# Kernel tuning notes

Hardware: AMD Instinct MI355X
Metric: run time of the kernel (lower is better)

The kernel has to match this reference:

```python
import jax, jax.numpy as jnp
import numpy as np

DIM = 256


def setup_inputs() -> dict:
    key = jax.random.key(0)
    ks = jax.random.split(key, 10)
    d = DIM
    inp = {
        "agent": jax.random.normal(ks[0], (64, d), dtype=jnp.float32),
        "x": jax.random.normal(ks[1], (8, 4096, d), dtype=jnp.float32),
        # parameters (stored as [in, out]; y = x @ W + b)
        "W_qkv": jax.random.normal(ks[2], (d, 3 * d), dtype=jnp.float32) * (d ** -0.5),
        "b_qkv": jnp.zeros((3 * d,), dtype=jnp.float32),
        "W_agent": jax.random.normal(ks[3], (d, 2 * d), dtype=jnp.float32) * (d ** -0.5),
        "b_agent": jnp.zeros((2 * d,), dtype=jnp.float32),
        "W_fc1": jax.random.normal(ks[4], (d, d), dtype=jnp.float32) * (d ** -0.5),
        "b_fc1": jnp.zeros((d,), dtype=jnp.float32),
        "W_fc2": jax.random.normal(ks[5], (d, d), dtype=jnp.float32) * (d ** -0.5),
        "b_fc2": jnp.zeros((d,), dtype=jnp.float32),
    }
    return inp


def reference(agent, x, W_qkv, b_qkv, W_agent, b_agent, W_fc1, b_fc1, W_fc2, b_fc2):
    d = x.shape[-1]
    scale = d ** -0.5
    # qkv projection of tokens: [B,N,3d] -> q,k,v each [B,N,d]
    qkv = x @ W_qkv + b_qkv
    q, k, v = jnp.split(qkv, 3, axis=-1)
    # agent projection: [K,2d] -> q_agent,k_agent each [K,d]
    ag = agent @ W_agent + b_agent
    q_agent, k_agent = jnp.split(ag, 2, axis=-1)
    # stage 1: agents attend over tokens -> [B,K,N]
    attn1 = jax.nn.softmax(jnp.einsum('kd,bnd->bkn', q_agent, k) * scale, axis=-1)
    va = jnp.einsum('bkn,bnd->bkd', attn1, v)  # [B,K,d]
    va = va @ W_fc1 + b_fc1
    # stage 2: tokens attend over agents -> [B,N,K]
    attn2 = jax.nn.softmax(jnp.einsum('bnd,kd->bnk', q, k_agent) * scale, axis=-1)
    out = jnp.einsum('bnk,bkd->bnd', attn2, va)  # [B,N,d]
    out = out @ W_fc2 + b_fc2
    return out + x
```

## Files before the change

### kernel.cpp

```cpp
#include <hip/hip_runtime.h>
#include <stdint.h>
#include <string.h>

#define BB 8
#define NN 4096
#define DD 256
#define QS 512
#define SCALE 0.0625f

using frag_ab = __attribute__((ext_vector_type(8))) short;
using frag_cd = __attribute__((ext_vector_type(4))) float;

__device__ __forceinline__ unsigned short f2bf(float f) {
    union { float f; unsigned u; } a; a.f = f;
    unsigned r = a.u + 0x7FFFu + ((a.u >> 16) & 1u);
    return (unsigned short)(r >> 16);
}

__global__ __launch_bounds__(256) void k_xconv(
    const float* __restrict__ x, unsigned short* __restrict__ xb)
{
    size_t idx = (size_t)blockIdx.x * 1024 + threadIdx.x * 4;
    float4 v = *(const float4*)&x[idx];
    unsigned short u[4] = {f2bf(v.x), f2bf(v.y), f2bf(v.z), f2bf(v.w)};
    uint2 pk; memcpy(&pk, u, 8);
    *(uint2*)&xb[idx] = pk;
}

__global__ __launch_bounds__(256) void k_setup(
    const float* __restrict__ Wqkv, unsigned short* __restrict__ Wt,
    const float* __restrict__ agent, const float* __restrict__ Wag,
    const float* __restrict__ bag, unsigned short* __restrict__ agb,
    const float* __restrict__ Wfc1, const float* __restrict__ Wfc2,
    const float* __restrict__ bfc1, float* __restrict__ W12, float* __restrict__ b12)
{
    __shared__ float sh[64 * 65];
    const int bx = blockIdx.x, tid = threadIdx.x;
    if (bx < 48) {
        const int n0 = (bx % 12) * 64, k0 = (bx / 12) * 64;
#pragma unroll
        for (int p = 0; p < 16; ++p) {
            int idx = p * 256 + tid;
            int k = idx >> 6, n = idx & 63;
            sh[k * 65 + n] = Wqkv[(k0 + k) * 768 + n0 + n];
        }
        __syncthreads();
#pragma unroll
        for (int p = 0; p < 16; ++p) {
            int idx = p * 256 + tid;
            int n = idx >> 6, k = idx & 63;
            Wt[(size_t)(n0 + n) * 256 + k0 + k] = f2bf(sh[k * 65 + n]);
        }
    } else if (bx < 112) {
        const int row = bx - 48;
        sh[tid] = agent[row * 256 + tid];
        __syncthreads();
#pragma unroll
        for (int h = 0; h < 2; ++h) {
            int j = tid + h * 256;
            float s = bag[j];
            for (int kk = 0; kk < 256; ++kk) s += sh[kk] * Wag[kk * 512 + j];
            agb[row * 512 + j] = f2bf(s);
        }
    } else {
        const int i = bx - 112, j = tid;
        float s = 0.f;
        for (int k = 0; k < 256; ++k) s += Wfc1[i * 256 + k] * Wfc2[k * 256 + j];
        W12[i * 256 + j] = s;
        if (i == 0) {
            float t = 0.f;
            for (int k = 0; k < 256; ++k) t += bfc1[k] * Wfc2[k * 256 + j];
            b12[j] = t;
        }
    }
}

__global__ __launch_bounds__(256) void k_qkv_mfma(
    const unsigned short* __restrict__ xb, const unsigned short* __restrict__ Wt,
    const float* __restrict__ bqkv, unsigned short* __restrict__ qkv,
    unsigned short* __restrict__ VT)
{
    __shared__ unsigned short lds[2 * 128 * 72];
    unsigned short* As = lds;
    unsigned short* Bs = lds + 128 * 72;
    const int m0 = blockIdx.x * 128;
    const int n0 = blockIdx.y * 128;
    const int tid = threadIdx.x;
    const int wave = tid >> 6, lane = tid & 63;
    const int ml = lane & 15, q = lane >> 4;
    const int wm = (wave & 1) * 64, wn = (wave >> 1) * 64;

    frag_cd acc[4][4];
#pragma unroll
    for (int i = 0; i < 4; ++i)
#pragma unroll
        for (int j = 0; j < 4; ++j)
#pragma unroll
            for (int r = 0; r < 4; ++r) acc[i][j][r] = 0.f;

    for (int kb = 0; kb < 256; kb += 64) {
        __syncthreads();
#pragma unroll
        for (int p = 0; p < 4; ++p) {
            int idx = p * 256 + tid;
            int r = idx >> 3, c = (idx & 7) * 8;
            *(uint4*)&As[r * 72 + c] =
                *(const uint4*)&xb[(size_t)(m0 + r) * 256 + kb + c];
            *(uint4*)&Bs[r * 72 + c] =
                *(const uint4*)&Wt[(size_t)(n0 + r) * 256 + kb + c];
        }
        __syncthreads();
#pragma unroll
        for (int ks = 0; ks < 2; ++ks) {
            const int kk = ks * 32 + q * 8;
            frag_ab a[4], b[4];
#pragma unroll
            for (int i = 0; i < 4; ++i)
                a[i] = *(const frag_ab*)&As[(wm + i * 16 + ml) * 72 + kk];
#pragma unroll
            for (int j = 0; j < 4; ++j)
                b[j] = *(const frag_ab*)&Bs[(wn + j * 16 + ml) * 72 + kk];
#pragma unroll
            for (int i = 0; i < 4; ++i)
#pragma unroll
                for (int j = 0; j < 4; ++j)
                    acc[i][j] = __builtin_amdgcn_mfma_f32_16x16x32_bf16(
                        a[i], b[j], acc[i][j], 0, 0, 0);
        }
    }

    float bias[4];
#pragma unroll
    for (int j = 0; j < 4; ++j) bias[j] = bqkv[n0 + wn + j * 16 + ml];

    if (n0 >= 512) {
        const int b = m0 >> 12;
        const int tok0 = (m0 & 4095) + wm;
        const int d0 = n0 - 512 + wn;
#pragma unroll
        for (int i = 0; i < 4; ++i)
#pragma unroll
            for (int j = 0; j < 4; ++j) {
                unsigned short u[4];
#pragma unroll
                for (int r = 0; r < 4; ++r) u[r] = f2bf(acc[i][j][r] + bias[j]);
                uint2 pk; memcpy(&pk, u, 8);
                *(uint2*)&VT[(size_t)(b * 256 + d0 + j * 16 + ml) * 4096 +
                             tok0 + i * 16 + q * 4] = pk;
            }
    } else {
        __syncthreads();
        unsigned short* E = lds + wave * 64 * 72;
#pragma unroll
        for (int i = 0; i < 4; ++i)
#pragma unroll
            for (int j = 0; j < 4; ++j)
#pragma unroll
                for (int r = 0; r < 4; ++r)
                    E[(i * 16 + q * 4 + r) * 72 + j * 16 + ml] =
                        f2bf(acc[i][j][r] + bias[j]);
        __syncthreads();
#pragma unroll
        for (int p = 0; p < 8; ++p) {
            int idx = p * 64 + lane;
            int r = idx >> 3, c = (idx & 7) * 8;
            *(uint4*)&qkv[(size_t)(m0 + wm + r) * QS + n0 + wn + c] =
                *(const uint4*)&E[r * 72 + c];
        }
    }
}

__global__ __launch_bounds__(256) void k_logits1_stats(
    const unsigned short* __restrict__ agb, const unsigned short* __restrict__ qkv,
    float* __restrict__ attn1, float* __restrict__ statM, float* __restrict__ statS)
{
    __shared__ unsigned short As[64 * 72];
    __shared__ unsigned short Bs[64 * 72];
    __shared__ float Sm[4][64], Ss[4][64], Cm[64];
    const int chunk = blockIdx.x;
    const int n0 = chunk * 64;
    const int b = blockIdx.y;
    const int tid = threadIdx.x;
    const int w = tid >> 6, lane = tid & 63;
    const int ml = lane & 15, q = lane >> 4;

    frag_cd acc[4];
#pragma unroll
    for (int j = 0; j < 4; ++j)
#pragma unroll
        for (int r = 0; r < 4; ++r) acc[j][r] = 0.f;

    for (int kb = 0; kb < 256; kb += 64) {
        __syncthreads();
#pragma unroll
        for (int p = 0; p < 2; ++p) {
            int idx = p * 256 + tid;
            int r = idx >> 3, c = (idx & 7) * 8;
            *(uint4*)&As[r * 72 + c] =
                *(const uint4*)&qkv[(size_t)(b * 4096 + n0 + r) * QS + 256 + kb + c];
            *(uint4*)&Bs[r * 72 + c] = *(const uint4*)&agb[r * 512 + kb + c];
        }
        __syncthreads();
#pragma unroll
        for (int ks = 0; ks < 2; ++ks) {
            const int kk = ks * 32 + q * 8;
            frag_ab a = *(const frag_ab*)&As[(w * 16 + ml) * 72 + kk];
#pragma unroll
            for (int j = 0; j < 4; ++j) {
                frag_ab bf = *(const frag_ab*)&Bs[(j * 16 + ml) * 72 + kk];
                acc[j] = __builtin_amdgcn_mfma_f32_16x16x32_bf16(a, bf, acc[j], 0, 0, 0);
            }
        }
    }

    float l[4][4];
#pragma unroll
    for (int j = 0; j < 4; ++j) {
        int ag = j * 16 + ml;
#pragma unroll
        for (int r = 0; r < 4; ++r) l[j][r] = acc[j][r] * SCALE;
        float4 o = make_float4(l[j][0], l[j][1], l[j][2], l[j][3]);
        *(float4*)&attn1[(size_t)(b * 64 + ag) * 4096 + n0 + w * 16 + q * 4] = o;
    }
#pragma unroll
    for (int j = 0; j < 4; ++j) {
        float m = fmaxf(fmaxf(l[j][0], l[j][1]), fmaxf(l[j][2], l[j][3]));
        m = fmaxf(m, __shfl_xor(m, 16));
        m = fmaxf(m, __shfl_xor(m, 32));
        if (q == 0) Sm[w][j * 16 + ml] = m;
    }
    __syncthreads();
    if (tid < 64)
        Cm[tid] = fmaxf(fmaxf(Sm[0][tid], Sm[1][tid]), fmaxf(Sm[2][tid], Sm[3][tid]));
    __syncthreads();
#pragma unroll
    for (int j = 0; j < 4; ++j) {
        float cm = Cm[j * 16 + ml];
        float s = __expf(l[j][0] - cm) + __expf(l[j][1] - cm) +
                  __expf(l[j][2] - cm) + __expf(l[j][3] - cm);
        s += __shfl_xor(s, 16);
        s += __shfl_xor(s, 32);
        if (q == 0) Ss[w][j * 16 + ml] = s;
    }
    __syncthreads();
    if (tid < 64) {
        float s = Ss[0][tid] + Ss[1][tid] + Ss[2][tid] + Ss[3][tid];
        size_t idx = (size_t)(b * 64 + tid) * 64 + chunk;
        statM[idx] = Cm[tid];
        statS[idx] = s;
    }
}

__global__ __launch_bounds__(256) void k_va_fused(
    const float* __restrict__ attn1, const float* __restrict__ statM,
    const float* __restrict__ statS, const unsigned short* __restrict__ VT,
    float* __restrict__ part)
{
    __shared__ unsigned short As[64 * 144];
    __shared__ unsigned short Bs[128 * 144];
    __shared__ float rowM[64], rowInv[64];
    const int s = blockIdx.x, dh = blockIdx.y, b = blockIdx.z;
    const int tid = threadIdx.x;
    const int w = tid >> 6, lane = tid & 63;
    const int ml = lane & 15, q = lane >> 4;

    if (tid < 64) {
        const float* pm = &statM[(size_t)(b * 64 + tid) * 64];
        const float* ps = &statS[(size_t)(b * 64 + tid) * 64];
        float m = -INFINITY;
#pragma unroll 8
        for (int c = 0; c < 64; ++c) m = fmaxf(m, pm[c]);
        float sum = 0.f;
#pragma unroll 8
        for (int c = 0; c < 64; ++c) sum += ps[c] * __expf(pm[c] - m);
        rowM[tid] = m;
        rowInv[tid] = 1.f / sum;
    }
#pragma unroll
    for (int p = 0; p < 8; ++p) {
        int idx = p * 256 + tid;
        int r = idx >> 4, c = (idx & 15) * 8;
        *(uint4*)&Bs[r * 144 + c] =
            *(const uint4*)&VT[(size_t)(b * 256 + dh * 128 + r) * 4096 + s * 128 + c];
    }
    __syncthreads();
#pragma unroll
    for (int p = 0; p < 32; ++p) {
        int idx = p * 256 + tid;
        int ag = idx >> 7, t = idx & 127;
        float l = attn1[(size_t)(b * 64 + ag) * 4096 + s * 128 + t];
        As[ag * 144 + t] = f2bf(__expf(l - rowM[ag]) * rowInv[ag]);
    }
    __syncthreads();

    frag_cd acc[4][2];
#pragma unroll
    for (int i = 0; i < 4; ++i)
#pragma unroll
        for (int j = 0; j < 2; ++j)
#pragma unroll
            for (int r = 0; r < 4; ++r) acc[i][j][r] = 0.f;
#pragma unroll
    for (int ks = 0; ks < 4; ++ks) {
        const int kk = ks * 32 + q * 8;
        frag_ab a[4];
#pragma unroll
        for (int i = 0; i < 4; ++i)
            a[i] = *(const frag_ab*)&As[(i * 16 + ml) * 144 + kk];
#pragma unroll
        for (int j = 0; j < 2; ++j) {
            frag_ab bf = *(const frag_ab*)&Bs[(w * 32 + j * 16 + ml) * 144 + kk];
#pragma unroll
            for (int i = 0; i < 4; ++i)
                acc[i][j] = __builtin_amdgcn_mfma_f32_16x16x32_bf16(
                    a[i], bf, acc[i][j], 0, 0, 0);
        }
    }
#pragma unroll
    for (int i = 0; i < 4; ++i)
#pragma unroll
        for (int j = 0; j < 2; ++j) {
            int d = dh * 128 + w * 32 + j * 16 + ml;
#pragma unroll
            for (int r = 0; r < 4; ++r)
                part[(size_t)((s * 8 + b) * 64 + i * 16 + q * 4 + r) * 256 + d] =
                    acc[i][j][r];
        }
}

__global__ __launch_bounds__(256) void k_fc(
    const float* __restrict__ part, const float* __restrict__ W12,
    const float* __restrict__ b12, unsigned short* __restrict__ va3t)
{
    __shared__ float rowb[256];
    const int row = blockIdx.x, tid = threadIdx.x;
    const int b = row >> 6, ag = row & 63;
    float sv = 0.f;
    for (int s = 0; s < 32; ++s)
        sv += part[(size_t)((s * 8 + b) * 64 + ag) * 256 + tid];
    rowb[tid] = sv;
    __syncthreads();
    float s2 = b12[tid];
    for (int k = 0; k < 256; ++k) s2 += rowb[k] * W12[k * 256 + tid];
    va3t[(size_t)(b * 256 + tid) * 64 + ag] = f2bf(s2);
}

__global__ __launch_bounds__(256) void k_stage2_mfma(
    const unsigned short* __restrict__ qkv, const unsigned short* __restrict__ agb,
    const unsigned short* __restrict__ va3t, const float* __restrict__ x,
    const float* __restrict__ bfc2, float* __restrict__ out)
{
    __shared__ unsigned short As[64 * 72];
    __shared__ unsigned short Bs[64 * 72];
    __shared__ unsigned short Vs[256 * 72];
    const int n0 = blockIdx.x * 64;
    const int b = blockIdx.y;
    const int tid = threadIdx.x;
    const int w = tid >> 6, lane = tid & 63;
    const int ml = lane & 15, q = lane >> 4;

#pragma unroll
    for (int p = 0; p < 8; ++p) {
        int idx = p * 256 + tid;
        int r = idx >> 3, c = (idx & 7) * 8;
        *(uint4*)&Vs[r * 72 + c] = *(const uint4*)&va3t[(size_t)(b * 256 + r) * 64 + c];
    }

    frag_cd acc1[4];
#pragma unroll
    for (int j = 0; j < 4; ++j)
#pragma unroll
        for (int r = 0; r < 4; ++r) acc1[j][r] = 0.f;

    for (int kb = 0; kb < 256; kb += 64) {
        __syncthreads();
#pragma unroll
        for (int p = 0; p < 2; ++p) {
            int idx = p * 256 + tid;
            int r = idx >> 3, c = (idx & 7) * 8;
            *(uint4*)&As[r * 72 + c] =
                *(const uint4*)&qkv[(size_t)(b * 4096 + n0 + r) * QS + kb + c];
            *(uint4*)&Bs[r * 72 + c] = *(const uint4*)&agb[r * 512 + 256 + kb + c];
        }
        __syncthreads();
#pragma unroll
        for (int ks = 0; ks < 2; ++ks) {
            const int kk = ks * 32 + q * 8;
            frag_ab a = *(const frag_ab*)&As[(w * 16 + ml) * 72 + kk];
#pragma unroll
            for (int j = 0; j < 4; ++j) {
                frag_ab bf = *(const frag_ab*)&Bs[(j * 16 + ml) * 72 + kk];
                acc1[j] = __builtin_amdgcn_mfma_f32_16x16x32_bf16(a, bf, acc1[j], 0, 0, 0);
            }
        }
    }

    unsigned short* Ps = As;
#pragma unroll
    for (int r = 0; r < 4; ++r) {
        float v0 = acc1[0][r] * SCALE, v1 = acc1[1][r] * SCALE;
        float v2 = acc1[2][r] * SCALE, v3 = acc1[3][r] * SCALE;
        float m = fmaxf(fmaxf(v0, v1), fmaxf(v2, v3));
#pragma unroll
        for (int mask = 1; mask <= 8; mask <<= 1) m = fmaxf(m, __shfl_xor(m, mask));
        float e0 = __expf(v0 - m), e1 = __expf(v1 - m);
        float e2 = __expf(v2 - m), e3 = __expf(v3 - m);
        float sm = e0 + e1 + e2 + e3;
#pragma unroll
        for (int mask = 1; mask <= 8; mask <<= 1) sm += __shfl_xor(sm, mask);
        float inv = 1.f / sm;
        int trow = w * 16 + q * 4 + r;
        Ps[trow * 72 + 0 * 16 + ml] = f2bf(e0 * inv);
        Ps[trow * 72 + 1 * 16 + ml] = f2bf(e1 * inv);
        Ps[trow * 72 + 2 * 16 + ml] = f2bf(e2 * inv);
        Ps[trow * 72 + 3 * 16 + ml] = f2bf(e3 * inv);
    }
    __syncthreads();

    frag_cd acc2[4][4];
#pragma unroll
    for (int i = 0; i < 4; ++i)
#pragma unroll
        for (int j = 0; j < 4; ++j)
#pragma unroll
            for (int r = 0; r < 4; ++r) acc2[i][j][r] = 0.f;
#pragma unroll
    for (int ks = 0; ks < 2; ++ks) {
        const int kk = ks * 32 + q * 8;
        frag_ab bf[4];
#pragma unroll
        for (int j = 0; j < 4; ++j)
            bf[j] = *(const frag_ab*)&Vs[(w * 64 + j * 16 + ml) * 72 + kk];
#pragma unroll
        for (int i = 0; i < 4; ++i) {
            frag_ab a = *(const frag_ab*)&Ps[(i * 16 + ml) * 72 + kk];
#pragma unroll
            for (int j = 0; j < 4; ++j)
                acc2[i][j] = __builtin_amdgcn_mfma_f32_16x16x32_bf16(
                    a, bf[j], acc2[i][j], 0, 0, 0);
        }
    }

    float bias[4];
#pragma unroll
    for (int j = 0; j < 4; ++j) bias[j] = bfc2[w * 64 + j * 16 + ml];
#pragma unroll
    for (int i = 0; i < 4; ++i) {
        size_t base = ((size_t)b * 4096 + n0 + i * 16 + q * 4) * 256;
#pragma unroll
        for (int j = 0; j < 4; ++j) {
            int d = w * 64 + j * 16 + ml;
#pragma unroll
            for (int r = 0; r < 4; ++r) {
                size_t a = base + (size_t)r * 256 + d;
                out[a] = acc2[i][j][r] + bias[j] + x[a];
            }
        }
    }
}

extern "C" void kernel_launch(void* const* d_in, const int* in_sizes, int n_in,
                              void* d_out, int out_size, void* d_ws, size_t ws_size,
                              hipStream_t stream) {
    const float* agent = (const float*)d_in[0];
    const float* x     = (const float*)d_in[1];
    const float* Wqkv  = (const float*)d_in[2];
    const float* bqkv  = (const float*)d_in[3];
    const float* Wag   = (const float*)d_in[4];
    const float* bag   = (const float*)d_in[5];
    const float* Wfc1  = (const float*)d_in[6];
    const float* bfc1  = (const float*)d_in[7];
    const float* Wfc2  = (const float*)d_in[8];
    const float* bfc2  = (const float*)d_in[9];
    float* out = (float*)d_out;

    char* w = (char*)d_ws;
    size_t off = 0;
    unsigned short* qkv = (unsigned short*)(w + off); off += (size_t)BB * NN * QS * 2;
    unsigned short* VT  = (unsigned short*)(w + off); off += (size_t)BB * DD * NN * 2;
    unsigned short* agb = (unsigned short*)(w + off); off += (size_t)64 * 512 * 2;
    float* attn1 = (float*)(w + off); off += (size_t)BB * 64 * NN * 4;
    float* statM = (float*)(w + off); off += (size_t)BB * 64 * 64 * 4;
    float* statS = (float*)(w + off); off += (size_t)BB * 64 * 64 * 4;
    float* W12 = (float*)(w + off); off += (size_t)256 * 256 * 4;
    float* b12 = (float*)(w + off); off += 4096;
    unsigned short* va3t = (unsigned short*)(w + off); off += (size_t)BB * DD * 64 * 2;
    unsigned short* Wt = (unsigned short*)(w + off); off += (size_t)768 * DD * 2;
    char* shared = w + off; off += (size_t)32 * BB * 64 * 256 * 4;
    unsigned short* xb = (unsigned short*)shared;
    float* part = (float*)shared;

    k_xconv<<<8192, 256, 0, stream>>>(x, xb);
    k_setup<<<368, 256, 0, stream>>>(Wqkv, Wt, agent, Wag, bag, agb,
                                     Wfc1, Wfc2, bfc1, W12, b12);
    k_qkv_mfma<<<dim3(256, 6), 256, 0, stream>>>(xb, Wt, bqkv, qkv, VT);
    k_logits1_stats<<<dim3(64, 8), 256, 0, stream>>>(agb, qkv, attn1, statM, statS);
    k_va_fused<<<dim3(32, 2, 8), 256, 0, stream>>>(attn1, statM, statS, VT, part);
    k_fc<<<512, 256, 0, stream>>>(part, W12, b12, va3t);
    k_stage2_mfma<<<dim3(64, 8), 256, 0, stream>>>(qkv, agb, va3t, x, bfc2, out);
}
```

Measured before the change: 199.3 us.

## Eliminate token QKV projection by folding weights into agent-side matrices

Rewrites the pipeline algebraically so the large x@W_qkv GEMM is never computed. Agent queries and keys are pre-multiplied by the q and k weight slices, giving one 128-column matrix that turns x directly into both attention logit sets. W_v is folded into fc1 and fc2, so stage 1 aggregates raw x. This removes the big projection and its q/k/v buffers, at the cost of a transposed bf16 copy of x and writing stage-2 logits to memory as fp32.

```diff
diff --git a/kernel.cpp b/kernel.cpp
--- a/kernel.cpp
+++ b/kernel.cpp
@@ -5,7 +5,6 @@
 #define BB 8
 #define NN 4096
 #define DD 256
-#define QS 512
 #define SCALE 0.0625f
 
 using frag_ab = __attribute__((ext_vector_type(8))) short;
@@ -17,178 +16,130 @@
     return (unsigned short)(r >> 16);
 }
 
-__global__ __launch_bounds__(256) void k_xconv(
-    const float* __restrict__ x, unsigned short* __restrict__ xb)
-{
-    size_t idx = (size_t)blockIdx.x * 1024 + threadIdx.x * 4;
-    float4 v = *(const float4*)&x[idx];
-    unsigned short u[4] = {f2bf(v.x), f2bf(v.y), f2bf(v.z), f2bf(v.w)};
-    uint2 pk; memcpy(&pk, u, 8);
-    *(uint2*)&xb[idx] = pk;
-}
-
-__global__ __launch_bounds__(256) void k_setup(
-    const float* __restrict__ Wqkv, unsigned short* __restrict__ Wt,
+__global__ __launch_bounds__(256) void k_xprep(
+    const float* __restrict__ x, unsigned short* __restrict__ xb,
+    unsigned short* __restrict__ xt)
+{
+    __shared__ float T[64 * 65];
+    const int n0 = blockIdx.x * 64, d0 = blockIdx.y * 64, b = blockIdx.z;
+    const int tid = threadIdx.x;
+#pragma unroll
+    for (int p = 0; p < 16; ++p) {
+        int idx = p * 256 + tid;
+        int n = idx >> 6, d = idx & 63;
+        T[n * 65 + d] = x[(size_t)(b * 4096 + n0 + n) * 256 + d0 + d];
+    }
+    __syncthreads();
+#pragma unroll
+    for (int p = 0; p < 16; ++p) {
+        int idx = p * 256 + tid;
+        int n = idx >> 6, d = idx & 63;
+        xb[(size_t)(b * 4096 + n0 + n) * 256 + d0 + d] = f2bf(T[n * 65 + d]);
+    }
+#pragma unroll
+    for (int p = 0; p < 16; ++p) {
+        int idx = p * 256 + tid;
+        int d = idx >> 6, n = idx & 63;
+        xt[(size_t)(b * 256 + d0 + d) * 4096 + n0 + n] = f2bf(T[n * 65 + d]);
+    }
+}
+
+__global__ __launch_bounds__(256) void k_setup1(
     const float* __restrict__ agent, const float* __restrict__ Wag,
-    const float* __restrict__ bag, unsigned short* __restrict__ agb,
-    const float* __restrict__ Wfc1, const float* __restrict__ Wfc2,
-    const float* __restrict__ bfc1, float* __restrict__ W12, float* __restrict__ b12)
-{
-    __shared__ float sh[64 * 65];
+    const float* __restrict__ bag, float* __restrict__ ag,
+    const float* __restrict__ Wqkv, const float* __restrict__ Wfc1,
+    const float* __restrict__ bqkv, const float* __restrict__ bfc1,
+    float* __restrict__ T, float* __restrict__ Tb)
+{
+    __shared__ float sh[256];
     const int bx = blockIdx.x, tid = threadIdx.x;
-    if (bx < 48) {
-        const int n0 = (bx % 12) * 64, k0 = (bx / 12) * 64;
-#pragma unroll
-        for (int p = 0; p < 16; ++p) {
-            int idx = p * 256 + tid;
-            int k = idx >> 6, n = idx & 63;
-            sh[k * 65 + n] = Wqkv[(k0 + k) * 768 + n0 + n];
-        }
-        __syncthreads();
-#pragma unroll
-        for (int p = 0; p < 16; ++p) {
-            int idx = p * 256 + tid;
-            int n = idx >> 6, k = idx & 63;
-            Wt[(size_t)(n0 + n) * 256 + k0 + k] = f2bf(sh[k * 65 + n]);
-        }
-    } else if (bx < 112) {
-        const int row = bx - 48;
-        sh[tid] = agent[row * 256 + tid];
+    if (bx < 64) {
+        sh[tid] = agent[bx * 256 + tid];
         __syncthreads();
 #pragma unroll
         for (int h = 0; h < 2; ++h) {
             int j = tid + h * 256;
             float s = bag[j];
             for (int kk = 0; kk < 256; ++kk) s += sh[kk] * Wag[kk * 512 + j];
-            agb[row * 512 + j] = f2bf(s);
+            ag[bx * 512 + j] = s;
         }
     } else {
-        const int i = bx - 112, j = tid;
+        const int i = bx - 64;
+        sh[tid] = Wqkv[i * 768 + 512 + tid];
+        __syncthreads();
         float s = 0.f;
-        for (int k = 0; k < 256; ++k) s += Wfc1[i * 256 + k] * Wfc2[k * 256 + j];
-        W12[i * 256 + j] = s;
+        for (int o = 0; o < 256; ++o) s += sh[o] * Wfc1[o * 256 + tid];
+        T[i * 256 + tid] = s;
+        if (i == 0) {
+            float t = bfc1[tid];
+            for (int o = 0; o < 256; ++o) t += bqkv[512 + o] * Wfc1[o * 256 + tid];
+            Tb[tid] = t;
+        }
+    }
+}
+
+__global__ __launch_bounds__(256) void k_setup2(
+    const float* __restrict__ ag, const float* __restrict__ Wqkv,
+    const float* __restrict__ bqkv, unsigned short* __restrict__ P12t,
+    float* __restrict__ c12, const float* __restrict__ T,
+    const float* __restrict__ Tb, const float* __restrict__ Wfc2,
+    float* __restrict__ W3, float* __restrict__ b3)
+{
+    __shared__ float arow[256];
+    __shared__ float red[256];
+    const int bx = blockIdx.x, tid = threadIdx.x;
+    if (bx < 128) {
+        const int c = bx;
+        const int woff = (c < 64) ? 256 : 0;
+        const int aoff = (c < 64) ? 0 : 256;
+        const int row = c & 63;
+        arow[tid] = ag[row * 512 + aoff + tid];
+        __syncthreads();
+        float s = 0.f;
+        for (int o = 0; o < 256; ++o) s += Wqkv[tid * 768 + woff + o] * arow[o];
+        P12t[(size_t)c * 256 + tid] = f2bf(SCALE * s);
+        red[tid] = bqkv[woff + tid] * arow[tid];
+        __syncthreads();
+        for (int st = 128; st; st >>= 1) {
+            if (tid < st) red[tid] += red[tid + st];
+            __syncthreads();
+        }
+        if (tid == 0) c12[c] = SCALE * red[0];
+    } else {
+        const int i = bx - 128;
+        arow[tid] = T[i * 256 + tid];
+        __syncthreads();
+        float s = 0.f;
+        for (int k = 0; k < 256; ++k) s += arow[k] * Wfc2[k * 256 + tid];
+        W3[i * 256 + tid] = s;
         if (i == 0) {
             float t = 0.f;
-            for (int k = 0; k < 256; ++k) t += bfc1[k] * Wfc2[k * 256 + j];
-            b12[j] = t;
-        }
-    }
-}
-
-__global__ __launch_bounds__(256) void k_qkv_mfma(
-    const unsigned short* __restrict__ xb, const unsigned short* __restrict__ Wt,
-    const float* __restrict__ bqkv, unsigned short* __restrict__ qkv,
-    unsigned short* __restrict__ VT)
-{
-    __shared__ unsigned short lds[2 * 128 * 72];
-    unsigned short* As = lds;
-    unsigned short* Bs = lds + 128 * 72;
-    const int m0 = blockIdx.x * 128;
-    const int n0 = blockIdx.y * 128;
-    const int tid = threadIdx.x;
-    const int wave = tid >> 6, lane = tid & 63;
-    const int ml = lane & 15, q = lane >> 4;
-    const int wm = (wave & 1) * 64, wn = (wave >> 1) * 64;
-
-    frag_cd acc[4][4];
-#pragma unroll
-    for (int i = 0; i < 4; ++i)
-#pragma unroll
-        for (int j = 0; j < 4; ++j)
-#pragma unroll
-            for (int r = 0; r < 4; ++r) acc[i][j][r] = 0.f;
-
-    for (int kb = 0; kb < 256; kb += 64) {
-        __syncthreads();
-#pragma unroll
-        for (int p = 0; p < 4; ++p) {
-            int idx = p * 256 + tid;
-            int r = idx >> 3, c = (idx & 7) * 8;
-            *(uint4*)&As[r * 72 + c] =
-                *(const uint4*)&xb[(size_t)(m0 + r) * 256 + kb + c];
-            *(uint4*)&Bs[r * 72 + c] =
-                *(const uint4*)&Wt[(size_t)(n0 + r) * 256 + kb + c];
-        }
-        __syncthreads();
-#pragma unroll
-        for (int ks = 0; ks < 2; ++ks) {
-            const int kk = ks * 32 + q * 8;
-            frag_ab a[4], b[4];
-#pragma unroll
-            for (int i = 0; i < 4; ++i)
-                a[i] = *(const frag_ab*)&As[(wm + i * 16 + ml) * 72 + kk];
-#pragma unroll
-            for (int j = 0; j < 4; ++j)
-                b[j] = *(const frag_ab*)&Bs[(wn + j * 16 + ml) * 72 + kk];
-#pragma unroll
-            for (int i = 0; i < 4; ++i)
-#pragma unroll
-                for (int j = 0; j < 4; ++j)
-                    acc[i][j] = __builtin_amdgcn_mfma_f32_16x16x32_bf16(
-                        a[i], b[j], acc[i][j], 0, 0, 0);
-        }
-    }
-
-    float bias[4];
-#pragma unroll
-    for (int j = 0; j < 4; ++j) bias[j] = bqkv[n0 + wn + j * 16 + ml];
-
-    if (n0 >= 512) {
-        const int b = m0 >> 12;
-        const int tok0 = (m0 & 4095) + wm;
-        const int d0 = n0 - 512 + wn;
-#pragma unroll
-        for (int i = 0; i < 4; ++i)
-#pragma unroll
-            for (int j = 0; j < 4; ++j) {
-                unsigned short u[4];
-#pragma unroll
-                for (int r = 0; r < 4; ++r) u[r] = f2bf(acc[i][j][r] + bias[j]);
-                uint2 pk; memcpy(&pk, u, 8);
-                *(uint2*)&VT[(size_t)(b * 256 + d0 + j * 16 + ml) * 4096 +
-                             tok0 + i * 16 + q * 4] = pk;
-            }
-    } else {
-        __syncthreads();
-        unsigned short* E = lds + wave * 64 * 72;
-#pragma unroll
-        for (int i = 0; i < 4; ++i)
-#pragma unroll
-            for (int j = 0; j < 4; ++j)
-#pragma unroll
-                for (int r = 0; r < 4; ++r)
-                    E[(i * 16 + q * 4 + r) * 72 + j * 16 + ml] =
-                        f2bf(acc[i][j][r] + bias[j]);
-        __syncthreads();
-#pragma unroll
-        for (int p = 0; p < 8; ++p) {
-            int idx = p * 64 + lane;
-            int r = idx >> 3, c = (idx & 7) * 8;
-            *(uint4*)&qkv[(size_t)(m0 + wm + r) * QS + n0 + wn + c] =
-                *(const uint4*)&E[r * 72 + c];
-        }
-    }
-}
-
-__global__ __launch_bounds__(256) void k_logits1_stats(
-    const unsigned short* __restrict__ agb, const unsigned short* __restrict__ qkv,
-    float* __restrict__ attn1, float* __restrict__ statM, float* __restrict__ statS)
+            for (int k = 0; k < 256; ++k) t += Tb[k] * Wfc2[k * 256 + tid];
+            b3[tid] = t;
+        }
+    }
+}
+
+__global__ __launch_bounds__(256) void k_logits(
+    const unsigned short* __restrict__ xb, const unsigned short* __restrict__ P12t,
+    const float* __restrict__ c12, float* __restrict__ l1, float* __restrict__ l2,
+    float* __restrict__ statM, float* __restrict__ statS)
 {
     __shared__ unsigned short As[64 * 72];
-    __shared__ unsigned short Bs[64 * 72];
-    __shared__ float Sm[4][64], Ss[4][64], Cm[64];
-    const int chunk = blockIdx.x;
+    __shared__ unsigned short Bs[128 * 72];
+    const int chunk = blockIdx.x, b = blockIdx.y;
     const int n0 = chunk * 64;
-    const int b = blockIdx.y;
     const int tid = threadIdx.x;
     const int w = tid >> 6, lane = tid & 63;
     const int ml = lane & 15, q = lane >> 4;
 
-    frag_cd acc[4];
-#pragma unroll
-    for (int j = 0; j < 4; ++j)
-#pragma unroll
-        for (int r = 0; r < 4; ++r) acc[j][r] = 0.f;
+    frag_cd acc[4][2];
+#pragma unroll
+    for (int i = 0; i < 4; ++i)
+#pragma unroll
+        for (int j = 0; j < 2; ++j)
+#pragma unroll
+            for (int r = 0; r < 4; ++r) acc[i][j][r] = 0.f;
 
     for (int kb = 0; kb < 256; kb += 64) {
         __syncthreads();
@@ -197,63 +148,88 @@
             int idx = p * 256 + tid;
             int r = idx >> 3, c = (idx & 7) * 8;
             *(uint4*)&As[r * 72 + c] =
-                *(const uint4*)&qkv[(size_t)(b * 4096 + n0 + r) * QS + 256 + kb + c];
-            *(uint4*)&Bs[r * 72 + c] = *(const uint4*)&agb[r * 512 + kb + c];
+                *(const uint4*)&xb[(size_t)(b * 4096 + n0 + r) * 256 + kb + c];
+        }
+#pragma unroll
+        for (int p = 0; p < 4; ++p) {
+            int idx = p * 256 + tid;
+            int r = idx >> 3, c = (idx & 7) * 8;
+            *(uint4*)&Bs[r * 72 + c] =
+                *(const uint4*)&P12t[(size_t)r * 256 + kb + c];
         }
         __syncthreads();
 #pragma unroll
         for (int ks = 0; ks < 2; ++ks) {
             const int kk = ks * 32 + q * 8;
-            frag_ab a = *(const frag_ab*)&As[(w * 16 + ml) * 72 + kk];
-#pragma unroll
-            for (int j = 0; j < 4; ++j) {
-                frag_ab bf = *(const frag_ab*)&Bs[(j * 16 + ml) * 72 + kk];
-                acc[j] = __builtin_amdgcn_mfma_f32_16x16x32_bf16(a, bf, acc[j], 0, 0, 0);
+            frag_ab a[4], bf[2];
+#pragma unroll
+            for (int i = 0; i < 4; ++i)
+                a[i] = *(const frag_ab*)&As[(i * 16 + ml) * 72 + kk];
+#pragma unroll
+            for (int j = 0; j < 2; ++j)
+                bf[j] = *(const frag_ab*)&Bs[(w * 32 + j * 16 + ml) * 72 + kk];
+#pragma unroll
+            for (int i = 0; i < 4; ++i)
+#pragma unroll
+                for (int j = 0; j < 2; ++j)
+                    acc[i][j] = __builtin_amdgcn_mfma_f32_16x16x32_bf16(
+                        a[i], bf[j], acc[i][j], 0, 0, 0);
+        }
+    }
+
+    float cc[2];
+#pragma unroll
+    for (int j = 0; j < 2; ++j) cc[j] = c12[w * 32 + j * 16 + ml];
+
+    if (w < 2) {
+#pragma unroll
+        for (int j = 0; j < 2; ++j) {
+            const int agc = w * 32 + j * 16 + ml;
+            float l[4][4];
+            float m = -INFINITY;
+#pragma unroll
+            for (int i = 0; i < 4; ++i)
+#pragma unroll
+                for (int r = 0; r < 4; ++r) {
+                    l[i][r] = acc[i][j][r] + cc[j];
+                    m = fmaxf(m, l[i][r]);
+                }
+            m = fmaxf(m, __shfl_xor(m, 16));
+            m = fmaxf(m, __shfl_xor(m, 32));
+            float s = 0.f;
+#pragma unroll
+            for (int i = 0; i < 4; ++i)
+#pragma unroll
+                for (int r = 0; r < 4; ++r) s += __expf(l[i][r] - m);
+            s += __shfl_xor(s, 16);
+            s += __shfl_xor(s, 32);
+            if (q == 0) {
+                size_t si = (size_t)(b * 64 + agc) * 64 + chunk;
+                statM[si] = m;
+                statS[si] = s;
             }
-        }
-    }
-
-    float l[4][4];
-#pragma unroll
-    for (int j = 0; j < 4; ++j) {
-        int ag = j * 16 + ml;
-#pragma unroll
-        for (int r = 0; r < 4; ++r) l[j][r] = acc[j][r] * SCALE;
-        float4 o = make_float4(l[j][0], l[j][1], l[j][2], l[j][3]);
-        *(float4*)&attn1[(size_t)(b * 64 + ag) * 4096 + n0 + w * 16 + q * 4] = o;
-    }
-#pragma unroll
-    for (int j = 0; j < 4; ++j) {
-        float m = fmaxf(fmaxf(l[j][0], l[j][1]), fmaxf(l[j][2], l[j][3]));
-        m = fmaxf(m, __shfl_xor(m, 16));
-        m = fmaxf(m, __shfl_xor(m, 32));
-        if (q == 0) Sm[w][j * 16 + ml] = m;
-    }
-    __syncthreads();
-    if (tid < 64)
-        Cm[tid] = fmaxf(fmaxf(Sm[0][tid], Sm[1][tid]), fmaxf(Sm[2][tid], Sm[3][tid]));
-    __syncthreads();
-#pragma unroll
-    for (int j = 0; j < 4; ++j) {
-        float cm = Cm[j * 16 + ml];
-        float s = __expf(l[j][0] - cm) + __expf(l[j][1] - cm) +
-                  __expf(l[j][2] - cm) + __expf(l[j][3] - cm);
-        s += __shfl_xor(s, 16);
-        s += __shfl_xor(s, 32);
-        if (q == 0) Ss[w][j * 16 + ml] = s;
-    }
-    __syncthreads();
-    if (tid < 64) {
-        float s = Ss[0][tid] + Ss[1][tid] + Ss[2][tid] + Ss[3][tid];
-        size_t idx = (size_t)(b * 64 + tid) * 64 + chunk;
-        statM[idx] = Cm[tid];
-        statS[idx] = s;
+#pragma unroll
+            for (int i = 0; i < 4; ++i)
+                *(float4*)&l1[(size_t)(b * 64 + agc) * 4096 + n0 + i * 16 + q * 4] =
+                    make_float4(l[i][0], l[i][1], l[i][2], l[i][3]);
+        }
+    } else {
+#pragma unroll
+        for (int j = 0; j < 2; ++j) {
+            const int agc = (w - 2) * 32 + j * 16 + ml;
+#pragma unroll
+            for (int i = 0; i < 4; ++i)
+#pragma unroll
+                for (int r = 0; r < 4; ++r)
+                    l2[(size_t)(b * 4096 + n0 + i * 16 + q * 4 + r) * 64 + agc] =
+                        acc[i][j][r] + cc[j];
+        }
     }
 }
 
 __global__ __launch_bounds__(256) void k_va_fused(
-    const float* __restrict__ attn1, const float* __restrict__ statM,
-    const float* __restrict__ statS, const unsigned short* __restrict__ VT,
+    const float* __restrict__ l1, const float* __restrict__ statM,
+    const float* __restrict__ statS, const unsigned short* __restrict__ xt,
     float* __restrict__ part)
 {
     __shared__ unsigned short As[64 * 144];
@@ -281,15 +257,15 @@
         int idx = p * 256 + tid;
         int r = idx >> 4, c = (idx & 15) * 8;
         *(uint4*)&Bs[r * 144 + c] =
-            *(const uint4*)&VT[(size_t)(b * 256 + dh * 128 + r) * 4096 + s * 128 + c];
+            *(const uint4*)&xt[(size_t)(b * 256 + dh * 128 + r) * 4096 + s * 128 + c];
     }
     __syncthreads();
 #pragma unroll
     for (int p = 0; p < 32; ++p) {
         int idx = p * 256 + tid;
-        int ag = idx >> 7, t = idx & 127;
-        float l = attn1[(size_t)(b * 64 + ag) * 4096 + s * 128 + t];
-        As[ag * 144 + t] = f2bf(__expf(l - rowM[ag]) * rowInv[ag]);
+        int agc = idx >> 7, t = idx & 127;
+        float l = l1[(size_t)(b * 64 + agc) * 4096 + s * 128 + t];
+        As[agc * 144 + t] = f2bf(__expf(l - rowM[agc]) * rowInv[agc]);
     }
     __syncthreads();
 
@@ -329,32 +305,30 @@
 }
 
 __global__ __launch_bounds__(256) void k_fc(
-    const float* __restrict__ part, const float* __restrict__ W12,
-    const float* __restrict__ b12, unsigned short* __restrict__ va3t)
+    const float* __restrict__ part, const float* __restrict__ W3,
+    const float* __restrict__ b3, unsigned short* __restrict__ va3t)
 {
     __shared__ float rowb[256];
     const int row = blockIdx.x, tid = threadIdx.x;
-    const int b = row >> 6, ag = row & 63;
+    const int b = row >> 6, agc = row & 63;
     float sv = 0.f;
     for (int s = 0; s < 32; ++s)
-        sv += part[(size_t)((s * 8 + b) * 64 + ag) * 256 + tid];
+        sv += part[(size_t)((s * 8 + b) * 64 + agc) * 256 + tid];
     rowb[tid] = sv;
     __syncthreads();
-    float s2 = b12[tid];
-    for (int k = 0; k < 256; ++k) s2 += rowb[k] * W12[k * 256 + tid];
-    va3t[(size_t)(b * 256 + tid) * 64 + ag] = f2bf(s2);
-}
-
-__global__ __launch_bounds__(256) void k_stage2_mfma(
-    const unsigned short* __restrict__ qkv, const unsigned short* __restrict__ agb,
-    const unsigned short* __restrict__ va3t, const float* __restrict__ x,
-    const float* __restrict__ bfc2, float* __restrict__ out)
-{
-    __shared__ unsigned short As[64 * 72];
-    __shared__ unsigned short Bs[64 * 72];
+    float s2 = b3[tid];
+    for (int k = 0; k < 256; ++k) s2 += rowb[k] * W3[k * 256 + tid];
+    va3t[(size_t)(b * 256 + tid) * 64 + agc] = f2bf(s2);
+}
+
+__global__ __launch_bounds__(256) void k_stage2(
+    const float* __restrict__ l2, const unsigned short* __restrict__ va3t,
+    const float* __restrict__ x, const float* __restrict__ bfc2,
+    float* __restrict__ out)
+{
+    __shared__ unsigned short Ps[64 * 72];
     __shared__ unsigned short Vs[256 * 72];
-    const int n0 = blockIdx.x * 64;
-    const int b = blockIdx.y;
+    const int n0 = blockIdx.x * 64, b = blockIdx.y;
     const int tid = threadIdx.x;
     const int w = tid >> 6, lane = tid & 63;
     const int ml = lane & 15, q = lane >> 4;
@@ -363,67 +337,46 @@
     for (int p = 0; p < 8; ++p) {
         int idx = p * 256 + tid;
         int r = idx >> 3, c = (idx & 7) * 8;
-        *(uint4*)&Vs[r * 72 + c] = *(const uint4*)&va3t[(size_t)(b * 256 + r) * 64 + c];
-    }
-
-    frag_cd acc1[4];
-#pragma unroll
-    for (int j = 0; j < 4; ++j)
-#pragma unroll
-        for (int r = 0; r < 4; ++r) acc1[j][r] = 0.f;
-
-    for (int kb = 0; kb < 256; kb += 64) {
-        __syncthreads();
-#pragma unroll
-        for (int p = 0; p < 2; ++p) {
-            int idx = p * 256 + tid;
-            int r = idx >> 3, c = (idx & 7) * 8;
-            *(uint4*)&As[r * 72 + c] =
-                *(const uint4*)&qkv[(size_t)(b * 4096 + n0 + r) * QS + kb + c];
-            *(uint4*)&Bs[r * 72 + c] = *(const uint4*)&agb[r * 512 + 256 + kb + c];
-        }
-        __syncthreads();
-#pragma unroll
-        for (int ks = 0; ks < 2; ++ks) {
-            const int kk = ks * 32 + q * 8;
-            frag_ab a = *(const frag_ab*)&As[(w * 16 + ml) * 72 + kk];
-#pragma unroll
-            for (int j = 0; j < 4; ++j) {
-                frag_ab bf = *(const frag_ab*)&Bs[(j * 16 + ml) * 72 + kk];
-                acc1[j] = __builtin_amdgcn_mfma_f32_16x16x32_bf16(a, bf, acc1[j], 0, 0, 0);
-            }
-        }
-    }
-
-    unsigned short* Ps = As;
-#pragma unroll
-    for (int r = 0; r < 4; ++r) {
-        float v0 = acc1[0][r] * SCALE, v1 = acc1[1][r] * SCALE;
-        float v2 = acc1[2][r] * SCALE, v3 = acc1[3][r] * SCALE;
-        float m = fmaxf(fmaxf(v0, v1), fmaxf(v2, v3));
-#pragma unroll
-        for (int mask = 1; mask <= 8; mask <<= 1) m = fmaxf(m, __shfl_xor(m, mask));
-        float e0 = __expf(v0 - m), e1 = __expf(v1 - m);
-        float e2 = __expf(v2 - m), e3 = __expf(v3 - m);
-        float sm = e0 + e1 + e2 + e3;
-#pragma unroll
-        for (int mask = 1; mask <= 8; mask <<= 1) sm += __shfl_xor(sm, mask);
-        float inv = 1.f / sm;
-        int trow = w * 16 + q * 4 + r;
-        Ps[trow * 72 + 0 * 16 + ml] = f2bf(e0 * inv);
-        Ps[trow * 72 + 1 * 16 + ml] = f2bf(e1 * inv);
-        Ps[trow * 72 + 2 * 16 + ml] = f2bf(e2 * inv);
-        Ps[trow * 72 + 3 * 16 + ml] = f2bf(e3 * inv);
+        *(uint4*)&Vs[r * 72 + c] =
+            *(const uint4*)&va3t[(size_t)(b * 256 + r) * 64 + c];
+    }
+
+    {
+        const int r = tid >> 2, c4 = tid & 3;
+        const float* lp = &l2[(size_t)(b * 4096 + n0 + r) * 64 + c4 * 16];
+        float v[16];
+#pragma unroll
+        for (int p = 0; p < 4; ++p) {
+            float4 f = *(const float4*)&lp[p * 4];
+            v[p * 4 + 0] = f.x; v[p * 4 + 1] = f.y;
+            v[p * 4 + 2] = f.z; v[p * 4 + 3] = f.w;
+        }
+        float m = -INFINITY;
+#pragma unroll
+        for (int i = 0; i < 16; ++i) m = fmaxf(m, v[i]);
+        m = fmaxf(m, __shfl_xor(m, 1));
+        m = fmaxf(m, __shfl_xor(m, 2));
+        float s = 0.f;
+#pragma unroll
+        for (int i = 0; i < 16; ++i) { v[i] = __expf(v[i] - m); s += v[i]; }
+        s += __shfl_xor(s, 1);
+        s += __shfl_xor(s, 2);
+        float inv = 1.f / s;
+        union { unsigned short u[16]; uint4 vec[2]; } pk;
+#pragma unroll
+        for (int i = 0; i < 16; ++i) pk.u[i] = f2bf(v[i] * inv);
+        *(uint4*)&Ps[r * 72 + c4 * 16] = pk.vec[0];
+        *(uint4*)&Ps[r * 72 + c4 * 16 + 8] = pk.vec[1];
     }
     __syncthreads();
 
-    frag_cd acc2[4][4];
+    frag_cd acc[4][4];
 #pragma unroll
     for (int i = 0; i < 4; ++i)
 #pragma unroll
         for (int j = 0; j < 4; ++j)
 #pragma unroll
-            for (int r = 0; r < 4; ++r) acc2[i][j][r] = 0.f;
+            for (int r = 0; r < 4; ++r) acc[i][j][r] = 0.f;
 #pragma unroll
     for (int ks = 0; ks < 2; ++ks) {
         const int kk = ks * 32 + q * 8;
@@ -436,8 +389,8 @@
             frag_ab a = *(const frag_ab*)&Ps[(i * 16 + ml) * 72 + kk];
 #pragma unroll
             for (int j = 0; j < 4; ++j)
-                acc2[i][j] = __builtin_amdgcn_mfma_f32_16x16x32_bf16(
-                    a, bf[j], acc2[i][j], 0, 0, 0);
+                acc[i][j] = __builtin_amdgcn_mfma_f32_16x16x32_bf16(
+                    a, bf[j], acc[i][j], 0, 0, 0);
         }
     }
 
@@ -453,7 +406,7 @@
 #pragma unroll
             for (int r = 0; r < 4; ++r) {
                 size_t a = base + (size_t)r * 256 + d;
-                out[a] = acc2[i][j][r] + bias[j] + x[a];
+                out[a] = acc[i][j][r] + bias[j] + x[a];
             }
         }
     }
@@ -476,26 +429,27 @@
 
     char* w = (char*)d_ws;
     size_t off = 0;
-    unsigned short* qkv = (unsigned short*)(w + off); off += (size_t)BB * NN * QS * 2;
-    unsigned short* VT  = (unsigned short*)(w + off); off += (size_t)BB * DD * NN * 2;
-    unsigned short* agb = (unsigned short*)(w + off); off += (size_t)64 * 512 * 2;
-    float* attn1 = (float*)(w + off); off += (size_t)BB * 64 * NN * 4;
+    unsigned short* xb   = (unsigned short*)(w + off); off += (size_t)BB * NN * DD * 2;
+    unsigned short* xt   = (unsigned short*)(w + off); off += (size_t)BB * DD * NN * 2;
+    float* ag   = (float*)(w + off); off += (size_t)64 * 512 * 4;
+    float* T    = (float*)(w + off); off += (size_t)256 * 256 * 4;
+    float* Tb   = (float*)(w + off); off += 256 * 4;
+    unsigned short* P12t = (unsigned short*)(w + off); off += (size_t)128 * 256 * 2;
+    float* c12  = (float*)(w + off); off += 128 * 4;
+    float* W3   = (float*)(w + off); off += (size_t)256 * 256 * 4;
+    float* b3   = (float*)(w + off); off += 256 * 4;
+    float* l1   = (float*)(w + off); off += (size_t)BB * 64 * NN * 4;
+    float* l2   = (float*)(w + off); off += (size_t)BB * NN * 64 * 4;
     float* statM = (float*)(w + off); off += (size_t)BB * 64 * 64 * 4;
     float* statS = (float*)(w + off); off += (size_t)BB * 64 * 64 * 4;
-    float* W12 = (float*)(w + off); off += (size_t)256 * 256 * 4;
-    float* b12 = (float*)(w + off); off += 4096;
+    float* part = (float*)(w + off); off += (size_t)32 * BB * 64 * 256 * 4;
     unsigned short* va3t = (unsigned short*)(w + off); off += (size_t)BB * DD * 64 * 2;
-    unsigned short* Wt = (unsigned short*)(w + off); off += (size_t)768 * DD * 2;
-    char* shared = w + off; off += (size_t)32 * BB * 64 * 256 * 4;
-    unsigned short* xb = (unsigned short*)shared;
-    float* part = (float*)shared;
-
-    k_xconv<<<8192, 256, 0, stream>>>(x, xb);
-    k_setup<<<368, 256, 0, stream>>>(Wqkv, Wt, agent, Wag, bag, agb,
-                                     Wfc1, Wfc2, bfc1, W12, b12);
-    k_qkv_mfma<<<dim3(256, 6), 256, 0, stream>>>(xb, Wt, bqkv, qkv, VT);
-    k_logits1_stats<<<dim3(64, 8), 256, 0, stream>>>(agb, qkv, attn1, statM, statS);
-    k_va_fused<<<dim3(32, 2, 8), 256, 0, stream>>>(attn1, statM, statS, VT, part);
-    k_fc<<<512, 256, 0, stream>>>(part, W12, b12, va3t);
-    k_stage2_mfma<<<dim3(64, 8), 256, 0, stream>>>(qkv, agb, va3t, x, bfc2, out);
-}
+
+    k_xprep<<<dim3(64, 4, BB), 256, 0, stream>>>(x, xb, xt);
+    k_setup1<<<320, 256, 0, stream>>>(agent, Wag, bag, ag, Wqkv, Wfc1, bqkv, bfc1, T, Tb);
+    k_setup2<<<384, 256, 0, stream>>>(ag, Wqkv, bqkv, P12t, c12, T, Tb, Wfc2, W3, b3);
+    k_logits<<<dim3(64, BB), 256, 0, stream>>>(xb, P12t, c12, l1, l2, statM, statS);
+    k_va_fused<<<dim3(32, 2, BB), 256, 0, stream>>>(l1, statM, statS, xt, part);
+    k_fc<<<512, 256, 0, stream>>>(part, W3, b3, va3t);
+    k_stage2<<<dim3(64, BB), 256, 0, stream>>>(l2, va3t, x, bfc2, out);
+}
```

After: 187.8 us. 1.06x faster.
